# Performance work log

Hardware: AMD Instinct MI355X
Metric: run time of the kernel (lower is better)

The kernel has to match this reference:

```python
import jax, jax.numpy as jnp
import numpy as np

N = 50000      # nodes
E = 800000     # edges (avg degree 16)
NFEAT = 256
NHID = 128
NCLASS = 40
NLAYERS_MID = 13  # gc2..gc14


def setup_inputs() -> dict:
    key = jax.random.key(0)
    ks = jax.random.split(key, 16)
    stdv_h = 1.0 / np.sqrt(NHID)     # GraphConvolution stdv = 1/sqrt(out_features)
    stdv_c = 1.0 / np.sqrt(NCLASS)
    u = lambda k, shape, s: jax.random.uniform(k, shape, jnp.float32, -s, s)
    return {
        "x": jax.random.normal(ks[0], (N, NFEAT), jnp.float32),
        "edge_src": jax.random.randint(ks[1], (E,), 0, N, jnp.int32),
        "edge_dst": jax.random.randint(ks[2], (E,), 0, N, jnp.int32),
        "edge_weight": jax.random.uniform(ks[3], (E,), jnp.float32),
        # skip-branch linear (self.weight / self.bias)
        "W0": u(ks[4], (NFEAT, NHID), stdv_h),
        "b0": u(ks[5], (NHID,), stdv_h),
        # gc1: nfeat -> nhid
        "W1": u(ks[6], (NFEAT, NHID), stdv_h),
        "b1": u(ks[7], (NHID,), stdv_h),
        # gc2..gc14: nhid -> nhid, stacked
        "Wmid": u(ks[8], (NLAYERS_MID, NHID, NHID), stdv_h),
        "bmid": u(ks[9], (NLAYERS_MID, NHID), stdv_h),
        # gc15: 14*nhid -> nclass
        "W15": u(ks[10], (14 * NHID, NCLASS), stdv_c),
        "b15": u(ks[11], (NCLASS,), stdv_c),
    }


def reference(x, edge_src, edge_dst, edge_weight, W0, b0, W1, b1, Wmid, bmid, W15, b15):
    n = x.shape[0]

    def gcn(h, W, b):
        # support = h @ W ; out = spmm(adj, support) + b  (adj as weighted edge list)
        support = h @ W
        msgs = support[edge_src] * edge_weight[:, None]           # [E, d]
        agg = jax.ops.segment_sum(msgs, edge_dst, num_segments=n)  # [N, d]
        return agg + b

    z = x @ W0 + b0
    x1 = jax.nn.relu(gcn(x, W1, b1)) + z

    def step(h, Wb):
        W, b = Wb
        hn = jax.nn.relu(gcn(h, W, b)) + h
        return hn, hn

    _, xs = jax.lax.scan(step, x1, (Wmid, bmid))   # xs: [13, N, NHID] = x2..x14
    all_x = jnp.concatenate([x1[None], xs], axis=0)  # [14, N, NHID] = x1..x14
    # concat order in torch code: (x14, x13, ..., x1)
    x_cat = jnp.swapaxes(all_x[::-1], 0, 1).reshape(n, 14 * NHID)
    # dropout is identity in eval mode
    x15 = gcn(x_cat, W15, b15)
    return jax.nn.log_softmax(x15, axis=1)
```

## Files before the change

### kernel.cpp

```cpp
#include <hip/hip_runtime.h>
#include <stdint.h>

#define NN 50000
#define EE 800000
#define DH 128
#define NC 40
#define KCAT (14*DH)
#define CAP 64

typedef __bf16 bf16x8 __attribute__((ext_vector_type(8)));
typedef float floatx4 __attribute__((ext_vector_type(4)));

#define GLOAD_LDS16(gp, lp)                                                          \
  __builtin_amdgcn_global_load_lds(                                                  \
      (const __attribute__((address_space(1))) uint32_t*)(gp),                       \
      (__attribute__((address_space(3))) uint32_t*)(lp), 16, 0, 0)

__device__ __forceinline__ float bf2f(unsigned short u) {
  union { uint32_t i; float f; } v; v.i = ((uint32_t)u) << 16; return v.f;
}
__device__ __forceinline__ unsigned short f2bf(float f) {
  union { float f; uint32_t i; } v; v.f = f;
  uint32_t x = v.i;
  uint32_t r = (x + 0x7fffu + ((x >> 16) & 1u)) >> 16;
  return (unsigned short)r;
}

__global__ void init_counts_detect(int* counts, int* hist, const unsigned short* xw) {
  int i = blockIdx.x * blockDim.x + threadIdx.x;
  if (i < NN) counts[i] = 0;
  if (i < 16) hist[i] = 0;
  if (blockIdx.x == 0) {
    int t = threadIdx.x;
    int wild = 0;
    for (int k = t; k < 4096; k += 256) {
      unsigned e = (xw[k] >> 7) & 0xFF;
      if (e >= 0x90) wild++;
    }
    __shared__ int red[256];
    red[t] = wild;
    __syncthreads();
    for (int s = 128; s > 0; s >>= 1) {
      if (t < s) red[t] += red[t + s];
      __syncthreads();
    }
    if (t == 0) counts[NN] = red[0];
  }
}

__global__ void convert_f4(const void* in, unsigned short* outp, int n4, const int* flag) {
  bool isf32 = (*flag) > 32;
  for (int i = blockIdx.x * blockDim.x + threadIdx.x; i < n4;
       i += gridDim.x * blockDim.x) {
    ushort4 o;
    if (isf32) {
      float4 v = ((const float4*)in)[i];
      o.x = f2bf(v.x); o.y = f2bf(v.y); o.z = f2bf(v.z); o.w = f2bf(v.w);
    } else {
      o = ((const ushort4*)in)[i];
    }
    ((ushort4*)outp)[i] = o;
  }
}

__global__ void convert_bias(const void* b0, const void* b1, const void* bm,
                             const void* b15, unsigned short* bb, const int* flag) {
  bool isf32 = (*flag) > 32;
  int i = blockIdx.x * blockDim.x + threadIdx.x;
  if (i >= 1960) return;
  const void* src; int off;
  if (i < 128)        { src = b0;  off = i; }
  else if (i < 256)   { src = b1;  off = i - 128; }
  else if (i < 1920)  { src = bm;  off = i - 256; }
  else                { src = b15; off = i - 1920; }
  bb[i] = isf32 ? f2bf(((const float*)src)[off]) : ((const unsigned short*)src)[off];
}

__global__ void transpose_w(const void* B, unsigned short* BT,
                            int L, int K, int M, int Mpad, const int* flag) {
  bool isf32 = (*flag) > 32;
  int total = L * Mpad * K;
  for (int idx = blockIdx.x * blockDim.x + threadIdx.x; idx < total;
       idx += gridDim.x * blockDim.x) {
    int k = idx % K;
    int n = (idx / K) % Mpad;
    int l = idx / (K * Mpad);
    unsigned short v = 0;
    if (n < M) {
      size_t si = (size_t)l * K * M + (size_t)k * M + n;
      v = isf32 ? f2bf(((const float*)B)[si]) : ((const unsigned short*)B)[si];
    }
    BT[idx] = v;
  }
}

__global__ void build_ell(const int* __restrict__ src, const int* __restrict__ dst,
                          const void* __restrict__ w,
                          int* __restrict__ cnt, int2* __restrict__ ell,
                          const int* __restrict__ flag) {
  bool isf32 = (*flag) > 32;
  int e = blockIdx.x * blockDim.x + threadIdx.x;
  if (e >= EE) return;
  int d = dst[e];
  if ((unsigned)d >= NN) return;
  int p = atomicAdd(&cnt[d], 1);
  if (p >= CAP) return;
  int s = src[e];
  float wf = isf32 ? ((const float*)w)[e] : bf2f(((const unsigned short*)w)[e]);
  if ((unsigned)s >= NN) { s = 0; wf = 0.f; }
  union { float f; int i; } wv; wv.f = wf;
  ell[(size_t)d * CAP + p] = make_int2(s, wv.i);
}

__global__ void pad_ell(const int* __restrict__ cnt, int2* __restrict__ ell) {
  int wave = threadIdx.x >> 6, lane = threadIdx.x & 63;
  int row = blockIdx.x * 4 + wave;
  if (row >= NN) return;
  int n = cnt[row];
  if (n > CAP) n = CAP;
  int padn = (n + 7) & ~7;
  if (lane >= n && lane < padn) ell[(size_t)row * CAP + lane] = make_int2(0, 0);
}

__global__ void hist_padn(const int* __restrict__ cnt, int* __restrict__ hist) {
  __shared__ int lh[9];
  int t = threadIdx.x;
  if (t < 9) lh[t] = 0;
  __syncthreads();
  int i = blockIdx.x * 256 + t;
  if (i < NN) {
    int n = cnt[i]; if (n > CAP) n = CAP;
    atomicAdd(&lh[(n + 7) >> 3], 1);
  }
  __syncthreads();
  if (t < 9 && lh[t]) atomicAdd(&hist[t], lh[t]);
}

__global__ void scan9(const int* __restrict__ hist, int* __restrict__ base) {
  if (threadIdx.x == 0) {
    int s = 0;
    for (int k = 0; k < 9; ++k) { base[k] = s; s += hist[k]; }
  }
}

__global__ void scatter_perm(const int* __restrict__ cnt, int* __restrict__ base,
                             int* __restrict__ perm) {
  __shared__ int lh[9], lbase[9];
  int t = threadIdx.x;
  if (t < 9) lh[t] = 0;
  __syncthreads();
  int i = blockIdx.x * 256 + t;
  int b = 0, p = 0;
  if (i < NN) {
    int n = cnt[i]; if (n > CAP) n = CAP;
    b = (n + 7) >> 3;
    p = atomicAdd(&lh[b], 1);
  }
  __syncthreads();
  if (t < 9) lbase[t] = lh[t] ? atomicAdd(&base[t], lh[t]) : 0;
  __syncthreads();
  if (i < NN) perm[lbase[b] + p] = i;
}

__global__ __launch_bounds__(256) void gemm_first(
    const unsigned short* __restrict__ A,
    const unsigned short* __restrict__ BT,
    unsigned short* __restrict__ C0,
    unsigned short* __restrict__ C1,
    const unsigned short* __restrict__ bias) {
  __shared__ unsigned short As[64 * 256];
  int t = threadIdx.x;
  int wave = t >> 6, lane = t & 63;
  int q = lane >> 4, mn = lane & 15;
  int r0 = blockIdx.x * 64;

  #pragma unroll
  for (int cc = 0; cc < 8; ++cc) {
    int L = cc * 4096 + t * 16;
    int row = L >> 9;
    int colb = (L & 511) ^ ((row & 7) << 4);
    int gr = r0 + row; if (gr >= NN) gr = NN - 1;
    GLOAD_LDS16((const char*)A + (size_t)gr * 512 + colb, (char*)As + L);
  }
  __syncthreads();

  floatx4 acc[4][4];
  floatx4 zf = {0.f, 0.f, 0.f, 0.f};
  #pragma unroll
  for (int i = 0; i < 4; ++i)
    #pragma unroll
    for (int j = 0; j < 4; ++j) acc[i][j] = zf;

  #pragma unroll
  for (int ks = 0; ks < 8; ++ks) {
    bf16x8 fa[4], fb[4];
    #pragma unroll
    for (int i = 0; i < 4; ++i) {
      int row = i * 16 + mn;
      fa[i] = *(const bf16x8*)((const char*)As + row * 512 +
                               ((ks * 64 + q * 16) ^ ((row & 7) << 4)));
    }
    #pragma unroll
    for (int j = 0; j < 4; ++j)
      fb[j] = *(const bf16x8*)((const char*)BT +
                               (size_t)(wave * 64 + j * 16 + mn) * 512 + ks * 64 + q * 16);
    #pragma unroll
    for (int i = 0; i < 4; ++i)
      #pragma unroll
      for (int j = 0; j < 4; ++j)
        acc[i][j] = __builtin_amdgcn_mfma_f32_16x16x32_bf16(fa[i], fb[j], acc[i][j], 0, 0, 0);
  }

  #pragma unroll
  for (int j = 0; j < 4; ++j) {
    int col = wave * 64 + j * 16 + mn;
    bool is0 = col < 128;
    int ccol = is0 ? col : col - 128;
    unsigned short* Cp = is0 ? C0 : C1;
    float badd = is0 ? bf2f(bias[ccol]) : 0.f;
    #pragma unroll
    for (int i = 0; i < 4; ++i) {
      int rbase = r0 + i * 16 + q * 4;
      #pragma unroll
      for (int rr = 0; rr < 4; ++rr) {
        int row = rbase + rr;
        if (row < NN) Cp[(size_t)row * 128 + ccol] = f2bf(acc[i][j][rr] + badd);
      }
    }
  }
}

__global__ __launch_bounds__(256) void gemm_mid(
    const unsigned short* __restrict__ A,
    const unsigned short* __restrict__ BT,
    unsigned short* __restrict__ C) {
  __shared__ unsigned short As[32 * 128];
  int t = threadIdx.x;
  int wave = t >> 6, lane = t & 63;
  int q = lane >> 4, mn = lane & 15;
  int r0 = blockIdx.x * 32;

  #pragma unroll
  for (int cc = 0; cc < 2; ++cc) {
    int L = cc * 4096 + t * 16;
    int row = L >> 8;
    int colb = (L & 255) ^ ((row & 7) << 4);
    int gr = r0 + row; if (gr >= NN) gr = NN - 1;
    GLOAD_LDS16((const char*)A + (size_t)gr * (KCAT * 2) + colb, (char*)As + L);
  }
  __syncthreads();

  floatx4 acc[2][2];
  floatx4 zf = {0.f, 0.f, 0.f, 0.f};
  #pragma unroll
  for (int i = 0; i < 2; ++i)
    #pragma unroll
    for (int j = 0; j < 2; ++j) acc[i][j] = zf;

  #pragma unroll
  for (int ks = 0; ks < 4; ++ks) {
    bf16x8 fa[2], fb[2];
    #pragma unroll
    for (int i = 0; i < 2; ++i) {
      int row = i * 16 + mn;
      fa[i] = *(const bf16x8*)((const char*)As + row * 256 +
                               ((ks * 64 + q * 16) ^ ((row & 7) << 4)));
    }
    #pragma unroll
    for (int j = 0; j < 2; ++j)
      fb[j] = *(const bf16x8*)((const char*)BT +
                               (size_t)(wave * 32 + j * 16 + mn) * 256 + ks * 64 + q * 16);
    #pragma unroll
    for (int i = 0; i < 2; ++i)
      #pragma unroll
      for (int j = 0; j < 2; ++j)
        acc[i][j] = __builtin_amdgcn_mfma_f32_16x16x32_bf16(fa[i], fb[j], acc[i][j], 0, 0, 0);
  }

  #pragma unroll
  for (int i = 0; i < 2; ++i) {
    int rbase = r0 + i * 16 + q * 4;
    #pragma unroll
    for (int j = 0; j < 2; ++j) {
      int col = wave * 32 + j * 16 + mn;
      #pragma unroll
      for (int rr = 0; rr < 4; ++rr) {
        int row = rbase + rr;
        if (row < NN) C[(size_t)row * 128 + col] = f2bf(acc[i][j][rr]);
      }
    }
  }
}

__global__ __launch_bounds__(256) void gemm_cat(
    const unsigned short* __restrict__ A, const unsigned short* __restrict__ BT ,
    float* __restrict__ C) {
  __shared__ unsigned short As[128][40];
  __shared__ unsigned short Bs[48][40];
  int t = threadIdx.x;
  int wave = t >> 6, lane = t & 63;
  int q = lane >> 4, mn = lane & 15;
  int r0 = blockIdx.x * 128;
  floatx4 acc[2][3];
  floatx4 zf = {0.f, 0.f, 0.f, 0.f};
  #pragma unroll
  for (int i = 0; i < 2; ++i)
    #pragma unroll
    for (int j = 0; j < 3; ++j) acc[i][j] = zf;

  int arow = t >> 2;
  int akc = (t & 3) << 3;

  for (int k0 = 0; k0 < KCAT; k0 += 32) {
    #pragma unroll
    for (int h = 0; h < 2; ++h) {
      int r = arow + h * 64;
      uint4 v = make_uint4(0, 0, 0, 0);
      if (r0 + r < NN) v = *(const uint4*)(A + (size_t)(r0 + r) * KCAT + k0 + akc);
      *(uint4*)(&As[r][akc]) = v;
    }
    if (t < 192) {
      uint4 v = *(const uint4*)(BT + (size_t)arow * KCAT + k0 + akc);
      *(uint4*)(&Bs[arow][akc]) = v;
    }
    __syncthreads();
    bf16x8 fa[2], fb[3];
    #pragma unroll
    for (int i = 0; i < 2; ++i) fa[i] = *(const bf16x8*)(&As[wave * 32 + i * 16 + mn][q * 8]);
    #pragma unroll
    for (int j = 0; j < 3; ++j) fb[j] = *(const bf16x8*)(&Bs[j * 16 + mn][q * 8]);
    #pragma unroll
    for (int i = 0; i < 2; ++i)
      #pragma unroll
      for (int j = 0; j < 3; ++j)
        acc[i][j] = __builtin_amdgcn_mfma_f32_16x16x32_bf16(fa[i], fb[j], acc[i][j], 0, 0, 0);
    __syncthreads();
  }
  #pragma unroll
  for (int i = 0; i < 2; ++i) {
    int rbase = r0 + wave * 32 + i * 16 + q * 4;
    #pragma unroll
    for (int j = 0; j < 3; ++j) {
      int col = j * 16 + mn;
      #pragma unroll
      for (int rr = 0; rr < 4; ++rr) {
        int row = rbase + rr;
        if (row < NN && col < NC) C[(size_t)row * NC + col] = acc[i][j][rr];
      }
    }
  }
}

__global__ __launch_bounds__(256) void spmm_layer4(
    const unsigned short* __restrict__ support, const int* __restrict__ cnt,
    const int2* __restrict__ ell, const int* __restrict__ perm,
    const unsigned short* __restrict__ bias,
    const unsigned short* __restrict__ res, int res_stride,
    unsigned short* __restrict__ out, int out_stride) {
  int t = threadIdx.x;
  int wave = t >> 6, lane = t & 63;
  int g = lane >> 4, gl = lane & 15;
  int rix = blockIdx.x * 16 + wave * 4 + g;
  int row = perm[rix];
  int n = cnt[row]; if (n > CAP) n = CAP;
  int padn = (n + 7) & ~7;
  const int2* erow = ell + (size_t)row * CAP;
  int2 ev0 = (gl      < padn) ? erow[gl]      : make_int2(0, 0);
  int2 ev1 = (gl + 16 < padn) ? erow[gl + 16] : make_int2(0, 0);
  int2 ev2 = (gl + 32 < padn) ? erow[gl + 32] : make_int2(0, 0);
  int2 ev3 = (gl + 48 < padn) ? erow[gl + 48] : make_int2(0, 0);
  int wmax = padn;
  wmax = max(wmax, __shfl_xor(wmax, 16));
  wmax = max(wmax, __shfl_xor(wmax, 32));
  int srcbase = lane & 0x30;
  int colb = gl * 16;

  float a[8];
  #pragma unroll
  for (int e = 0; e < 8; ++e) a[e] = 0.f;
  uint4 gA[4], gB[4];

  auto load4 = [&](uint4* gbuf, int2 EV, int off) {
    #pragma unroll
    for (int u = 0; u < 4; ++u) {
      int s = __shfl(EV.x, srcbase + off + u);
      gbuf[u] = *(const uint4*)((const char*)support + (size_t)s * 256 + colb);
    }
  };
  auto fma4 = [&](const uint4* gbuf, int2 EV, int off) {
    #pragma unroll
    for (int u = 0; u < 4; ++u) {
      union { int i; float f; } wv; wv.i = __shfl(EV.y, srcbase + off + u);
      uint32_t w[4] = {gbuf[u].x, gbuf[u].y, gbuf[u].z, gbuf[u].w};
      #pragma unroll
      for (int e = 0; e < 4; ++e) {
        union { uint32_t i; float f; } lo, hi;
        lo.i = w[e] << 16;
        hi.i = w[e] & 0xffff0000u;
        a[2 * e]     += wv.f * lo.f;
        a[2 * e + 1] += wv.f * hi.f;
      }
    }
  };

  if (wmax > 0) {
    load4(gA, ev0, 0);
                     load4(gB, ev0, 4);                    fma4(gA, ev0, 0);
     { if (wmax >  8) load4(gA, ev0, 8);                   fma4(gB, ev0, 4); }
    if (wmax >  8) { if (wmax > 12) load4(gB, ev0, 12);           fma4(gA, ev0, 8); }
    if (wmax > 12) { if (wmax > 16) load4(gA, ev1, 0);            fma4(gB, ev0, 12); }
    if (wmax > 16) { if (wmax > 20) load4(gB, ev1, 4);            fma4(gA, ev1, 0); }
    if (wmax > 20) { if (wmax > 24) load4(gA, ev1, 8);            fma4(gB, ev1, 4); }
    if (wmax > 24) { if (wmax > 28) load4(gB, ev1, 12);           fma4(gA, ev1, 8); }
    if (wmax > 28) { if (wmax > 32) load4(gA, ev2, 0);            fma4(gB, ev1, 12); }
    if (wmax > 32) { if (wmax > 36) load4(gB, ev2, 4);            fma4(gA, ev2, 0); }
    if (wmax > 36) { if (wmax > 40) load4(gA, ev2, 8);            fma4(gB, ev2, 4); }
    if (wmax > 40) { if (wmax > 44) load4(gB, ev2, 12);           fma4(gA, ev2, 8); }
    if (wmax > 44) { if (wmax > 48) load4(gA, ev3, 0);            fma4(gB, ev2, 12); }
    if (wmax > 48) { if (wmax > 52) load4(gB, ev3, 4);            fma4(gA, ev3, 0); }
    if (wmax > 52) { if (wmax > 56) load4(gA, ev3, 8);            fma4(gB, ev3, 4); }
    if (wmax > 56) { if (wmax > 60) load4(gB, ev3, 12);           fma4(gA, ev3, 8); }
    if (wmax > 60) fma4(gB, ev3, 12);
  }

  uint4 bw = *(const uint4*)((const char*)bias + colb);
  uint4 rw = *(const uint4*)((const char*)res + (size_t)row * res_stride * 2 + colb);
  uint32_t bwa[4] = {bw.x, bw.y, bw.z, bw.w};
  uint32_t rwa[4] = {rw.x, rw.y, rw.z, rw.w};
  uint32_t ob[4];
  #pragma unroll
  for (int e = 0; e < 4; ++e) {
    union { uint32_t i; float f; } blo, bhi, rlo, rhi;
    blo.i = bwa[e] << 16; bhi.i = bwa[e] & 0xffff0000u;
    rlo.i = rwa[e] << 16; rhi.i = rwa[e] & 0xffff0000u;
    float v0 = fmaxf(a[2 * e] + blo.f, 0.f) + rlo.f;
    float v1 = fmaxf(a[2 * e + 1] + bhi.f, 0.f) + rhi.f;
    ob[e] = (uint32_t)f2bf(v0) | ((uint32_t)f2bf(v1) << 16);
  }
  uint4 ov = make_uint4(ob[0], ob[1], ob[2], ob[3]);
  *(uint4*)((char*)out + (size_t)row * out_stride * 2 + colb) = ov;
}

__global__ __launch_bounds__(256) void spmm_softmax_out(
    const float* __restrict__ s15, const int* __restrict__ cnt,
    const int2* __restrict__ ell, const unsigned short* __restrict__ bias,
    float* __restrict__ out) {
  int wave = threadIdx.x >> 6, lane = threadIdx.x & 63;
  int row = blockIdx.x * 4 + wave;
  if (row >= NN) return;
  int n = cnt[row];
  if (n > CAP) n = CAP;
  int padn = (n + 7) & ~7;
  int2 ev = make_int2(0, 0);
  if (lane < padn) ev = ell[(size_t)row * CAP + lane];
  int fl = lane < NC ? lane : NC - 1;
  float acc = 0.f;
  for (int j = 0; j < padn; j += 4) {
    float g[4];
    #pragma unroll
    for (int u = 0; u < 4; ++u) {
      int s = __shfl(ev.x, j + u);
      g[u] = s15[(size_t)s * NC + fl];
    }
    #pragma unroll
    for (int u = 0; u < 4; ++u) {
      union { int i; float f; } wv; wv.i = __shfl(ev.y, j + u);
      acc += wv.f * g[u];
    }
  }
  acc += bf2f(bias[fl]);
  float v = (lane < NC) ? acc : -3.0e38f;
  float m = v;
  #pragma unroll
  for (int off = 32; off > 0; off >>= 1) m = fmaxf(m, __shfl_xor(m, off));
  float e = (lane < NC) ? expf(v - m) : 0.f;
  float sum = e;
  #pragma unroll
  for (int off = 32; off > 0; off >>= 1) sum += __shfl_xor(sum, off);
  if (lane < NC) out[(size_t)row * NC + lane] = v - m - logf(sum);
}

extern "C" void kernel_launch(void* const* d_in, const int* in_sizes, int n_in,
                              void* d_out, int out_size, void* d_ws, size_t ws_size,
                              hipStream_t stream) {
  const void* x   = d_in[0];
  const int* esrc = (const int*)d_in[1];
  const int* edst = (const int*)d_in[2];
  const void* ew  = d_in[3];
  const void* W0  = d_in[4];
  const void* b0  = d_in[5];
  const void* W1  = d_in[6];
  const void* b1  = d_in[7];
  const void* Wm  = d_in[8];
  const void* bm  = d_in[9];
  const void* W15 = d_in[10];
  const void* b15 = d_in[11];
  float* out = (float*)d_out;

  char* ws = (char*)d_ws;
  size_t off = 0;
  auto alloc = [&](size_t bytes) -> void* {
    void* p = ws + off;
    off = (off + bytes + 255) & ~(size_t)255;
    return p;
  };
  unsigned short* xcat = (unsigned short*)alloc((size_t)NN * KCAT * 2);
  unsigned short* xbf  = (unsigned short*)alloc((size_t)NN * 256 * 2);
  unsigned short* supp = (unsigned short*)alloc((size_t)NN * DH * 2);
  unsigned short* zbuf = (unsigned short*)alloc((size_t)NN * DH * 2);
  float* s15           = (float*)alloc((size_t)NN * NC * 4);
  int* counts          = (int*)alloc((size_t)(NN + 1) * 4);
  int* perm            = (int*)alloc((size_t)NN * 4);
  int* hist            = (int*)alloc(64);
  int* hbase           = (int*)alloc(64);
  int2* ell            = (int2*)alloc((size_t)NN * CAP * 8);
  unsigned short* W01T = (unsigned short*)alloc((size_t)256 * 256 * 2);
  unsigned short* WmT  = (unsigned short*)alloc((size_t)13 * 128 * 128 * 2);
  unsigned short* W15T = (unsigned short*)alloc((size_t)48 * 1792 * 2);
  unsigned short* bb   = (unsigned short*)alloc((size_t)(128 + 128 + 13 * 128 + 40) * 2);
  if (off > ws_size) return;
  int* flag = counts + NN;
  unsigned short* b0b  = bb;
  unsigned short* b1b  = bb + 128;
  unsigned short* bmb  = bb + 256;
  unsigned short* b15b = bb + 256 + 13 * 128;

  init_counts_detect<<<197, 256, 0, stream>>>(counts, hist, (const unsigned short*)x);
  transpose_w<<<128, 256, 0, stream>>>(W0, W01T, 1, 256, 128, 128, flag);
  transpose_w<<<128, 256, 0, stream>>>(W1, W01T + 128 * 256, 1, 256, 128, 128, flag);
  transpose_w<<<832, 256, 0, stream>>>(Wm, WmT, 13, 128, 128, 128, flag);
  transpose_w<<<336, 256, 0, stream>>>(W15, W15T, 1, 1792, 40, 48, flag);
  convert_f4<<<2048, 256, 0, stream>>>(x, xbf, NN * 256 / 4, flag);
  convert_bias<<<8, 256, 0, stream>>>(b0, b1, bm, b15, bb, flag);
  build_ell<<<3125, 256, 0, stream>>>(esrc, edst, ew, counts, ell, flag);

  int gb64  = (NN + 63) / 64;
  int gb32  = (NN + 31) / 32;
  int gb128 = (NN + 127) / 128;
  int sb    = (NN + 3) / 4;
  int pb    = (NN + 255) / 256;
  int s4b   = NN / 16;
  pad_ell<<<sb, 256, 0, stream>>>(counts, ell);
  hist_padn<<<pb, 256, 0, stream>>>(counts, hist);
  scan9<<<1, 64, 0, stream>>>(hist, hbase);
  scatter_perm<<<pb, 256, 0, stream>>>(counts, hbase, perm);
  gemm_first<<<gb64, 256, 0, stream>>>(xbf, W01T, zbuf, supp, b0b);
  spmm_layer4<<<s4b, 256, 0, stream>>>(supp, counts, ell, perm, b1b, zbuf, DH,
                                       xcat + 13 * DH, KCAT);
  for (int l = 0; l < 13; ++l) {
    gemm_mid<<<gb32, 256, 0, stream>>>(xcat + (13 - l) * DH,
                                       WmT + l * 128 * 128, supp);
    spmm_layer4<<<s4b, 256, 0, stream>>>(supp, counts, ell, perm, bmb + l * DH,
                                         xcat + (13 - l) * DH, KCAT,
                                         xcat + (12 - l) * DH, KCAT);
  }
  gemm_cat<<<gb128, 256, 0, stream>>>(xcat, W15T, s15);
  spmm_softmax_out<<<sb, 256, 0, stream>>>(s15, counts, ell, b15b, out);
}
```

Baseline: 949.5 us.

## Split SpMM feature columns into four slices across blocks with nontemporal I/O

The SpMM layer kernel now launches four blocks per 16-row group, and each block handles a 64-byte slice of the 128 feature columns. A lane now loads 4 bytes per neighbour row instead of 16. This gives four times as many blocks and fewer registers per thread, which should raise occupancy and memory-level parallelism for the gather. In exchange, each ELL row and perm entry is read four times, and the per-lane gathers are narrower, less coalesced accesses. Edge-list, residual loads and output stores also switch to nontemporal loads and stores to reduce cache pollution.

```diff
diff --git a/kernel.cpp b/kernel.cpp
--- a/kernel.cpp
+++ b/kernel.cpp
@@ -351,94 +351,92 @@
   }
 }
 
-__global__ __launch_bounds__(256) void spmm_layer4(
+__global__ __launch_bounds__(256) void spmm_slice(
     const unsigned short* __restrict__ support, const int* __restrict__ cnt,
     const int2* __restrict__ ell, const int* __restrict__ perm,
     const unsigned short* __restrict__ bias,
     const unsigned short* __restrict__ res, int res_stride,
     unsigned short* __restrict__ out, int out_stride) {
+  int bid = blockIdx.x;
+  int slice = bid & 3;
+  int rblk = bid >> 2;
   int t = threadIdx.x;
   int wave = t >> 6, lane = t & 63;
   int g = lane >> 4, gl = lane & 15;
-  int rix = blockIdx.x * 16 + wave * 4 + g;
+  int rix = rblk * 16 + wave * 4 + g;
   int row = perm[rix];
   int n = cnt[row]; if (n > CAP) n = CAP;
   int padn = (n + 7) & ~7;
-  const int2* erow = ell + (size_t)row * CAP;
-  int2 ev0 = (gl      < padn) ? erow[gl]      : make_int2(0, 0);
-  int2 ev1 = (gl + 16 < padn) ? erow[gl + 16] : make_int2(0, 0);
-  int2 ev2 = (gl + 32 < padn) ? erow[gl + 32] : make_int2(0, 0);
-  int2 ev3 = (gl + 48 < padn) ? erow[gl + 48] : make_int2(0, 0);
+  const unsigned long long* erow =
+      (const unsigned long long*)(ell + (size_t)row * CAP);
+  unsigned long long e0 = 0, e1 = 0, e2 = 0, e3 = 0;
+  if (gl      < padn) e0 = __builtin_nontemporal_load(erow + gl);
+  if (gl + 16 < padn) e1 = __builtin_nontemporal_load(erow + gl + 16);
+  if (gl + 32 < padn) e2 = __builtin_nontemporal_load(erow + gl + 32);
+  if (gl + 48 < padn) e3 = __builtin_nontemporal_load(erow + gl + 48);
+  int2 ev0 = make_int2((int)e0, (int)(e0 >> 32));
+  int2 ev1 = make_int2((int)e1, (int)(e1 >> 32));
+  int2 ev2 = make_int2((int)e2, (int)(e2 >> 32));
+  int2 ev3 = make_int2((int)e3, (int)(e3 >> 32));
   int wmax = padn;
   wmax = max(wmax, __shfl_xor(wmax, 16));
   wmax = max(wmax, __shfl_xor(wmax, 32));
   int srcbase = lane & 0x30;
-  int colb = gl * 16;
-
-  float a[8];
-  #pragma unroll
-  for (int e = 0; e < 8; ++e) a[e] = 0.f;
-  uint4 gA[4], gB[4];
-
-  auto load4 = [&](uint4* gbuf, int2 EV, int off) {
+  int colb = slice * 64 + gl * 4;
+
+  float a0 = 0.f, a1 = 0.f;
+  uint32_t gA[4], gB[4];
+
+  auto load4 = [&](uint32_t* gbuf, int2 EV, int off) {
     #pragma unroll
     for (int u = 0; u < 4; ++u) {
       int s = __shfl(EV.x, srcbase + off + u);
-      gbuf[u] = *(const uint4*)((const char*)support + (size_t)s * 256 + colb);
+      gbuf[u] = *(const uint32_t*)((const char*)support + (size_t)s * 256 + colb);
     }
   };
-  auto fma4 = [&](const uint4* gbuf, int2 EV, int off) {
+  auto fma4 = [&](const uint32_t* gbuf, int2 EV, int off) {
     #pragma unroll
     for (int u = 0; u < 4; ++u) {
       union { int i; float f; } wv; wv.i = __shfl(EV.y, srcbase + off + u);
-      uint32_t w[4] = {gbuf[u].x, gbuf[u].y, gbuf[u].z, gbuf[u].w};
-      #pragma unroll
-      for (int e = 0; e < 4; ++e) {
-        union { uint32_t i; float f; } lo, hi;
-        lo.i = w[e] << 16;
-        hi.i = w[e] & 0xffff0000u;
-        a[2 * e]     += wv.f * lo.f;
-        a[2 * e + 1] += wv.f * hi.f;
-      }
+      union { uint32_t i; float f; } lo, hi;
+      lo.i = gbuf[u] << 16;
+      hi.i = gbuf[u] & 0xffff0000u;
+      a0 += wv.f * lo.f;
+      a1 += wv.f * hi.f;
     }
   };
 
   if (wmax > 0) {
     load4(gA, ev0, 0);
-                     load4(gB, ev0, 4);                    fma4(gA, ev0, 0);
-     { if (wmax >  8) load4(gA, ev0, 8);                   fma4(gB, ev0, 4); }
-    if (wmax >  8) { if (wmax > 12) load4(gB, ev0, 12);           fma4(gA, ev0, 8); }
-    if (wmax > 12) { if (wmax > 16) load4(gA, ev1, 0);            fma4(gB, ev0, 12); }
-    if (wmax > 16) { if (wmax > 20) load4(gB, ev1, 4);            fma4(gA, ev1, 0); }
-    if (wmax > 20) { if (wmax > 24) load4(gA, ev1, 8);            fma4(gB, ev1, 4); }
-    if (wmax > 24) { if (wmax > 28) load4(gB, ev1, 12);           fma4(gA, ev1, 8); }
-    if (wmax > 28) { if (wmax > 32) load4(gA, ev2, 0);            fma4(gB, ev1, 12); }
-    if (wmax > 32) { if (wmax > 36) load4(gB, ev2, 4);            fma4(gA, ev2, 0); }
-    if (wmax > 36) { if (wmax > 40) load4(gA, ev2, 8);            fma4(gB, ev2, 4); }
-    if (wmax > 40) { if (wmax > 44) load4(gB, ev2, 12);           fma4(gA, ev2, 8); }
-    if (wmax > 44) { if (wmax > 48) load4(gA, ev3, 0);            fma4(gB, ev2, 12); }
-    if (wmax > 48) { if (wmax > 52) load4(gB, ev3, 4);            fma4(gA, ev3, 0); }
-    if (wmax > 52) { if (wmax > 56) load4(gA, ev3, 8);            fma4(gB, ev3, 4); }
-    if (wmax > 56) { if (wmax > 60) load4(gB, ev3, 12);           fma4(gA, ev3, 8); }
+    load4(gB, ev0, 4);                                  fma4(gA, ev0, 0);
+    { if (wmax >  8) load4(gA, ev0, 8);                 fma4(gB, ev0, 4); }
+    if (wmax >  8) { if (wmax > 12) load4(gB, ev0, 12); fma4(gA, ev0, 8); }
+    if (wmax > 12) { if (wmax > 16) load4(gA, ev1, 0);  fma4(gB, ev0, 12); }
+    if (wmax > 16) { if (wmax > 20) load4(gB, ev1, 4);  fma4(gA, ev1, 0); }
+    if (wmax > 20) { if (wmax > 24) load4(gA, ev1, 8);  fma4(gB, ev1, 4); }
+    if (wmax > 24) { if (wmax > 28) load4(gB, ev1, 12); fma4(gA, ev1, 8); }
+    if (wmax > 28) { if (wmax > 32) load4(gA, ev2, 0);  fma4(gB, ev1, 12); }
+    if (wmax > 32) { if (wmax > 36) load4(gB, ev2, 4);  fma4(gA, ev2, 0); }
+    if (wmax > 36) { if (wmax > 40) load4(gA, ev2, 8);  fma4(gB, ev2, 4); }
+    if (wmax > 40) { if (wmax > 44) load4(gB, ev2, 12); fma4(gA, ev2, 8); }
+    if (wmax > 44) { if (wmax > 48) load4(gA, ev3, 0);  fma4(gB, ev2, 12); }
+    if (wmax > 48) { if (wmax > 52) load4(gB, ev3, 4);  fma4(gA, ev3, 0); }
+    if (wmax > 52) { if (wmax > 56) load4(gA, ev3, 8);  fma4(gB, ev3, 4); }
+    if (wmax > 56) { if (wmax > 60) load4(gB, ev3, 12); fma4(gA, ev3, 8); }
     if (wmax > 60) fma4(gB, ev3, 12);
   }
 
-  uint4 bw = *(const uint4*)((const char*)bias + colb);
-  uint4 rw = *(const uint4*)((const char*)res + (size_t)row * res_stride * 2 + colb);
-  uint32_t bwa[4] = {bw.x, bw.y, bw.z, bw.w};
-  uint32_t rwa[4] = {rw.x, rw.y, rw.z, rw.w};
-  uint32_t ob[4];
-  #pragma unroll
-  for (int e = 0; e < 4; ++e) {
-    union { uint32_t i; float f; } blo, bhi, rlo, rhi;
-    blo.i = bwa[e] << 16; bhi.i = bwa[e] & 0xffff0000u;
-    rlo.i = rwa[e] << 16; rhi.i = rwa[e] & 0xffff0000u;
-    float v0 = fmaxf(a[2 * e] + blo.f, 0.f) + rlo.f;
-    float v1 = fmaxf(a[2 * e + 1] + bhi.f, 0.f) + rhi.f;
-    ob[e] = (uint32_t)f2bf(v0) | ((uint32_t)f2bf(v1) << 16);
-  }
-  uint4 ov = make_uint4(ob[0], ob[1], ob[2], ob[3]);
-  *(uint4*)((char*)out + (size_t)row * out_stride * 2 + colb) = ov;
+  uint32_t bw = *(const uint32_t*)((const char*)bias + colb);
+  uint32_t rw = __builtin_nontemporal_load(
+      (const uint32_t*)((const char*)res + (size_t)row * res_stride * 2 + colb));
+  union { uint32_t i; float f; } blo, bhi, rlo, rhi;
+  blo.i = bw << 16; bhi.i = bw & 0xffff0000u;
+  rlo.i = rw << 16; rhi.i = rw & 0xffff0000u;
+  float v0 = fmaxf(a0 + blo.f, 0.f) + rlo.f;
+  float v1 = fmaxf(a1 + bhi.f, 0.f) + rhi.f;
+  uint32_t o = (uint32_t)f2bf(v0) | ((uint32_t)f2bf(v1) << 16);
+  __builtin_nontemporal_store(
+      o, (uint32_t*)((char*)out + (size_t)row * out_stride * 2 + colb));
 }
 
 __global__ __launch_bounds__(256) void spmm_softmax_out(
@@ -539,20 +537,20 @@
   int gb128 = (NN + 127) / 128;
   int sb    = (NN + 3) / 4;
   int pb    = (NN + 255) / 256;
-  int s4b   = NN / 16;
+  int ssb   = (NN / 16) * 4;
   pad_ell<<<sb, 256, 0, stream>>>(counts, ell);
   hist_padn<<<pb, 256, 0, stream>>>(counts, hist);
   scan9<<<1, 64, 0, stream>>>(hist, hbase);
   scatter_perm<<<pb, 256, 0, stream>>>(counts, hbase, perm);
   gemm_first<<<gb64, 256, 0, stream>>>(xbf, W01T, zbuf, supp, b0b);
-  spmm_layer4<<<s4b, 256, 0, stream>>>(supp, counts, ell, perm, b1b, zbuf, DH,
-                                       xcat + 13 * DH, KCAT);
+  spmm_slice<<<ssb, 256, 0, stream>>>(supp, counts, ell, perm, b1b, zbuf, DH,
+                                      xcat + 13 * DH, KCAT);
   for (int l = 0; l < 13; ++l) {
     gemm_mid<<<gb32, 256, 0, stream>>>(xcat + (13 - l) * DH,
                                        WmT + l * 128 * 128, supp);
-    spmm_layer4<<<s4b, 256, 0, stream>>>(supp, counts, ell, perm, bmb + l * DH,
-                                         xcat + (13 - l) * DH, KCAT,
-                                         xcat + (12 - l) * DH, KCAT);
+    spmm_slice<<<ssb, 256, 0, stream>>>(supp, counts, ell, perm, bmb + l * DH,
+                                        xcat + (13 - l) * DH, KCAT,
+                                        xcat + (12 - l) * DH, KCAT);
   }
   gemm_cat<<<gb128, 256, 0, stream>>>(xcat, W15T, s15);
   spmm_softmax_out<<<sb, 256, 0, stream>>>(s15, counts, ell, b15b, out);
```

Result: slower. 1.181 ms (+24.4%).
